# Kernel optimization log

Measured on AMD Instinct MI355X. Metric: run time of the kernel, lower is better.

Reference implementation:

```python
import jax, jax.numpy as jnp
import numpy as np
from jax import lax

B, S, W, V, E = 128, 128, 16, 128, 32
FILTERS = [256, 256, 256]
KS = [2, 3, 4]
NC = 10
EPS = 1e-5


def setup_inputs() -> dict:
    key = jax.random.key(0)
    ks = jax.random.split(key, 16)
    idx = jax.random.randint(ks[0], (B, S, W), 0, V)
    x = jax.nn.one_hot(idx, V, dtype=jnp.float32)  # [B,S,W,V] one-hot chars
    in_ch = E * W
    d = {"x": x, "emb_w": jax.random.normal(ks[1], (V, E), jnp.float32) * 0.05}
    for i, (f, k) in enumerate(zip(FILTERS, KS)):
        d[f"conv_w{i}"] = jax.random.normal(ks[2 + i], (f, in_ch, k), jnp.float32) * 0.02
        d[f"conv_b{i}"] = jnp.zeros((f,), jnp.float32)
        d[f"bn_g{i}"] = jnp.ones((f,), jnp.float32)
        d[f"bn_b{i}"] = jnp.zeros((f,), jnp.float32)
    d["fc1_w"] = jax.random.normal(ks[10], (sum(FILTERS), 100), jnp.float32) * 0.02
    d["fc1_b"] = jnp.zeros((100,), jnp.float32)
    d["bn1_g"] = jnp.ones((100,), jnp.float32)
    d["bn1_b"] = jnp.zeros((100,), jnp.float32)
    d["fc2_w"] = jax.random.normal(ks[11], (100, NC), jnp.float32) * 0.02
    d["fc2_b"] = jnp.zeros((NC,), jnp.float32)
    return d


def _bn(h, g, b, axes):
    # training-mode batchnorm with biased variance (matches torch BatchNorm math)
    mu = jnp.mean(h, axis=axes, keepdims=True)
    var = jnp.mean(jnp.square(h - mu), axis=axes, keepdims=True)
    shp = [1] * h.ndim
    shp[1] = h.shape[1]
    return (h - mu) * lax.rsqrt(var + EPS) * g.reshape(shp) + b.reshape(shp)


def _forward(x, emb_w, conv_ws, conv_bs, bn_gs, bn_bs, fc1_w, fc1_b, bn1_g, bn1_b, fc2_w, fc2_b):
    b, s, w, v = x.shape
    # one-hot bmm embedding == dense projection; flatten word_len*embed per word
    emb = jnp.einsum('bswv,ve->bswe', x, emb_w).reshape(b, s, w * emb_w.shape[1])
    h = emb.transpose(0, 2, 1)  # [B, W*E, S]
    pooled = []
    for cw, cb, g, bb in zip(conv_ws, conv_bs, bn_gs, bn_bs):
        c = lax.conv_general_dilated(h, cw, (1,), 'VALID',
                                     dimension_numbers=('NCH', 'OIH', 'NCH'))
        c = c + cb[None, :, None]
        c = jax.nn.relu(_bn(c, g, bb, axes=(0, 2)))
        pooled.append(jnp.max(c, axis=2))  # global max pool over length
    z = jnp.concatenate(pooled, axis=1)  # [B, sum(filters)]
    z = z @ fc1_w + fc1_b
    z = jax.nn.relu(_bn2d(z, bn1_g, bn1_b))
    # dropout is identity in eval mode
    return jax.nn.softmax(z @ fc2_w + fc2_b, axis=1)


def _bn2d(h, g, b):
    mu = jnp.mean(h, axis=0, keepdims=True)
    var = jnp.mean(jnp.square(h - mu), axis=0, keepdims=True)
    return (h - mu) * lax.rsqrt(var + EPS) * g[None, :] + b[None, :]


def reference(x, emb_w, conv_w0, conv_b0, bn_g0, bn_b0, conv_w1, conv_b1, bn_g1, bn_b1,
              conv_w2, conv_b2, bn_g2, bn_b2, fc1_w, fc1_b, bn1_g, bn1_b, fc2_w, fc2_b):
    return _forward(x, emb_w,
                    [conv_w0, conv_w1, conv_w2], [conv_b0, conv_b1, conv_b2],
                    [bn_g0, bn_g1, bn_g2], [bn_b0, bn_b1, bn_b2],
                    fc1_w, fc1_b, bn1_g, bn1_b, fc2_w, fc2_b)
```

## Files before the change

kernel.cpp:

```cpp
#include <hip/hip_runtime.h>
#include <cstdint>
#include <cstddef>

#define MTOT 16384
#define MPAD 16388
#define INCH 512
#define NF   256
#define PREPB 6144

typedef __attribute__((ext_vector_type(4))) float f32x4;
typedef __attribute__((ext_vector_type(8))) short bf16x8;

__device__ __forceinline__ short f2bf(float f) {
    union { float f; unsigned u; } v; v.f = f;
    unsigned r = v.u + 0x7FFFu + ((v.u >> 16) & 1u);
    return (short)(r >> 16);
}

__device__ __forceinline__ void gld16(const short* g, short* l) {
    __builtin_amdgcn_global_load_lds(
        (const __attribute__((address_space(1))) unsigned int*)g,
        (__attribute__((address_space(3))) unsigned int*)l,
        16, 0, 0);
}

__global__ void embed_prep(const float* __restrict__ x, const float* __restrict__ ew,
                           short* __restrict__ emb,
                           const float* __restrict__ w0, const float* __restrict__ w1,
                           const float* __restrict__ w2, short* __restrict__ Wtb) {
    int tid = threadIdx.x;
    if (blockIdx.x < PREPB) {
        int blk = blockIdx.x;
        int conv = blk >> 11;
        int ki = conv + 2;
        int K = 512 * ki;
        int idx = (blk & 2047) * 256 + tid;
        if (idx >= K * NF) return;
        int u = idx >> 9;
        int ic = idx & 511;
        int f = u / ki;
        int j = u - f * ki;
        const float* w = (conv == 0) ? w0 : (conv == 1) ? w1 : w2;
        float val = w[(size_t)f * K + ic * ki + j];
        int k = j * 512 + ic;
        int kt = k >> 6, kl = k & 63;
        int kc = kl >> 3, klo = kl & 7;
        int nb = f >> 7, fr = f & 127;
        int cc = kc ^ (fr & 7);
        size_t off = (conv == 0) ? 0 : (conv == 1) ? 262144 : 655360;
        Wtb[off + (((size_t)(kt * 2 + nb) * 128 + fr) * 8 + cc) * 8 + klo] = f2bf(val);
        return;
    }
    int m = blockIdx.x - PREPB;
    if (m >= MTOT) {
        if (tid < 64) {
            uint4 z = make_uint4(0u, 0u, 0u, 0u);
            *(uint4*)&emb[(size_t)m * INCH + tid * 8] = z;
        }
        return;
    }
    int w = tid >> 4, u = tid & 15;
    const float* xr = x + ((size_t)m * 16 + w) * 128 + u * 8;
    float4 a0 = *(const float4*)xr;
    float4 a1 = *(const float4*)(xr + 4);
    float vals[8] = {a0.x, a0.y, a0.z, a0.w, a1.x, a1.y, a1.z, a1.w};
    int myidx = 0;
#pragma unroll
    for (int jj = 0; jj < 8; ++jj)
        if (vals[jj] != 0.f) myidx = u * 8 + jj;
#pragma unroll
    for (int off = 1; off < 16; off <<= 1)
        myidx = max(myidx, __shfl_xor(myidx, off));
    if (u < 4) {
        const float* er = ew + (size_t)myidx * 32 + u * 8;
        float4 e0 = *(const float4*)er;
        float4 e1 = *(const float4*)(er + 4);
        short h[8];
        h[0] = f2bf(e0.x); h[1] = f2bf(e0.y); h[2] = f2bf(e0.z); h[3] = f2bf(e0.w);
        h[4] = f2bf(e1.x); h[5] = f2bf(e1.y); h[6] = f2bf(e1.z); h[7] = f2bf(e1.w);
        *(uint4*)&emb[(size_t)m * INCH + w * 32 + u * 8] = *(uint4*)h;
    }
}

__launch_bounds__(256)
__global__ void conv_gemm(const short* __restrict__ emb, const short* __restrict__ Wtb,
                          const float* __restrict__ cb0, const float* __restrict__ cb1,
                          const float* __restrict__ cb2,
                          float* __restrict__ sumP, float* __restrict__ ssqP,
                          float* __restrict__ mxF, float* __restrict__ mnF) {
    int o = blockIdx.x;
    int logical = (o & 7) * 96 + (o >> 3);
    int mb = logical / 6;
    int r6 = logical - mb * 6;
    int conv = r6 >> 1;
    int nb = r6 & 1;
    int ki = conv + 2;
    int m0 = mb * 128;
    const short* Wc = Wtb + ((conv == 0) ? 0 : (conv == 1) ? 262144 : 655360);

    __shared__ __align__(16) short As[128 * 64];
    __shared__ __align__(16) short Bs[128 * 64];

    int tid = threadIdx.x;
    int wv = tid >> 6, lane = tid & 63, g = lane >> 4, ln = lane & 15;
    int wr = wv >> 1, wc = wv & 1;

    f32x4 acc[4][4];
#pragma unroll
    for (int i = 0; i < 4; ++i)
#pragma unroll
        for (int n = 0; n < 4; ++n) acc[i][n] = (f32x4){0.f, 0.f, 0.f, 0.f};

    int arow[4], acol[4];
#pragma unroll
    for (int q = 0; q < 4; ++q) {
        int c = q * 256 + tid;
        arow[q] = c >> 3;
        acol[q] = ((c & 7) ^ (arow[q] & 7)) * 8;
    }
    int aOff[2][4], bOff[2][4];
#pragma unroll
    for (int kk = 0; kk < 2; ++kk)
#pragma unroll
        for (int i = 0; i < 4; ++i) {
            int R = wr * 64 + i * 16 + ln;
            aOff[kk][i] = R * 64 + (((kk * 4 + g) ^ (R & 7)) * 8);
            int F = wc * 64 + i * 16 + ln;
            bOff[kk][i] = F * 64 + (((kk * 4 + g) ^ (F & 7)) * 8);
        }

    for (int j = 0; j < ki; ++j) {
        const short* embj = emb + (size_t)(m0 + j) * INCH;
        for (int ic0 = 0; ic0 < INCH; ic0 += 64) {
            int kt = j * 8 + (ic0 >> 6);
            const short* Bsrc = Wc + (size_t)(kt * 2 + nb) * 8192;
            __syncthreads();
#pragma unroll
            for (int q = 0; q < 4; ++q) {
                gld16(embj + (size_t)arow[q] * INCH + ic0 + acol[q],
                      As + q * 2048 + wv * 512);
                gld16(Bsrc + (q * 256 + tid) * 8,
                      Bs + q * 2048 + wv * 512);
            }
            __syncthreads();
#pragma unroll
            for (int kk = 0; kk < 2; ++kk) {
                bf16x8 afr[4], bfr[4];
#pragma unroll
                for (int mi = 0; mi < 4; ++mi) afr[mi] = *(const bf16x8*)&As[aOff[kk][mi]];
#pragma unroll
                for (int ni = 0; ni < 4; ++ni) bfr[ni] = *(const bf16x8*)&Bs[bOff[kk][ni]];
#pragma unroll
                for (int mi = 0; mi < 4; ++mi)
#pragma unroll
                    for (int ni = 0; ni < 4; ++ni)
                        acc[mi][ni] = __builtin_amdgcn_mfma_f32_16x16x32_bf16(afr[mi], bfr[ni], acc[mi][ni], 0, 0, 0);
            }
        }
    }

    int L = 127 - conv;
    const float* cbp = (conv == 0) ? cb0 : (conv == 1) ? cb1 : cb2;
    float s[4] = {0.f, 0.f, 0.f, 0.f}, q[4] = {0.f, 0.f, 0.f, 0.f};
    float mx[4], mn[4], cb[4];
#pragma unroll
    for (int ni = 0; ni < 4; ++ni) {
        mx[ni] = -3.0e38f; mn[ni] = 3.0e38f;
        cb[ni] = cbp[nb * 128 + wc * 64 + ni * 16 + ln];
    }
#pragma unroll
    for (int mi = 0; mi < 4; ++mi) {
#pragma unroll
        for (int r = 0; r < 4; ++r) {
            int t = wr * 64 + mi * 16 + g * 4 + r;
            if (t >= L) continue;
#pragma unroll
            for (int ni = 0; ni < 4; ++ni) {
                float c = acc[mi][ni][r] + cb[ni];
                s[ni] += c; q[ni] += c * c;
                mx[ni] = fmaxf(mx[ni], c); mn[ni] = fminf(mn[ni], c);
            }
        }
    }
#pragma unroll
    for (int off = 16; off < 64; off <<= 1) {
#pragma unroll
        for (int ni = 0; ni < 4; ++ni) {
            s[ni] += __shfl_xor(s[ni], off);
            q[ni] += __shfl_xor(q[ni], off);
            mx[ni] = fmaxf(mx[ni], __shfl_xor(mx[ni], off));
            mn[ni] = fminf(mn[ni], __shfl_xor(mn[ni], off));
        }
    }
    __syncthreads();
    float* sm = (float*)As;
    if (g == 0) {
#pragma unroll
        for (int ni = 0; ni < 4; ++ni) {
            int col = wc * 64 + ni * 16 + ln;
            int oo = wr * 128 + col;
            sm[oo] = s[ni]; sm[256 + oo] = q[ni];
            sm[512 + oo] = mx[ni]; sm[768 + oo] = mn[ni];
        }
    }
    __syncthreads();
    if (tid < 128) {
        float S  = sm[tid] + sm[128 + tid];
        float Q  = sm[256 + tid] + sm[384 + tid];
        float MX = fmaxf(sm[512 + tid], sm[640 + tid]);
        float MN = fminf(sm[768 + tid], sm[896 + tid]);
        size_t off2 = ((size_t)(conv * 128 + mb)) * 256 + nb * 128 + tid;
        sumP[off2] = S; ssqP[off2] = Q; mxF[off2] = MX; mnF[off2] = MN;
    }
}

__global__ void bn_stats(const float* __restrict__ sumP, const float* __restrict__ ssqP,
                         const float* __restrict__ g0, const float* __restrict__ g1,
                         const float* __restrict__ g2,
                         const float* __restrict__ b0, const float* __restrict__ b1,
                         const float* __restrict__ b2,
                         float* __restrict__ af, float* __restrict__ df) {
    int conv = blockIdx.x;
    int tid = threadIdx.x;
    int part = tid >> 8, f = tid & 255;
    float s = 0.f, q = 0.f;
#pragma unroll 4
    for (int mb = part * 32; mb < part * 32 + 32; ++mb) {
        size_t o = ((size_t)(conv * 128 + mb)) * 256 + f;
        s += sumP[o]; q += ssqP[o];
    }
    __shared__ float sred[4][256], qred[4][256];
    sred[part][f] = s; qred[part][f] = q;
    __syncthreads();
    if (part == 0) {
        s = sred[0][f] + sred[1][f] + sred[2][f] + sred[3][f];
        q = qred[0][f] + qred[1][f] + qred[2][f] + qred[3][f];
        int L = 127 - conv;
        float n = 128.f * (float)L;
        float mu = s / n;
        float var = fmaxf(q / n - mu * mu, 0.f);
        const float* gp = (conv == 0) ? g0 : (conv == 1) ? g1 : g2;
        const float* bp = (conv == 0) ? b0 : (conv == 1) ? b1 : b2;
        float a = gp[f] * rsqrtf(var + 1e-5f);
        af[conv * 256 + f] = a;
        df[conv * 256 + f] = bp[f] - mu * a;
    }
}

__global__ void pool_fc1(const float* __restrict__ mxF, const float* __restrict__ mnF,
                         const float* __restrict__ af, const float* __restrict__ df,
                         const float* __restrict__ fc1w, const float* __restrict__ fc1b,
                         float* __restrict__ zb) {
    int b = blockIdx.x;
    int tid = threadIdx.x;
    __shared__ float pl[768];
    __shared__ float ps[8][100];
    if (tid < 768) {
        int conv = tid >> 8, f = tid & 255;
        size_t o = ((size_t)(conv * 128 + b)) * 256 + f;
        float a = af[tid], d = df[tid];
        float v = (a >= 0.f) ? mxF[o] : mnF[o];
        pl[tid] = fmaxf(a * v + d, 0.f);
    }
    __syncthreads();
    if (tid < 800) {
        int part = tid / 100, f = tid % 100;
        const float* pp = pl + part * 96;
        const float* wp = fc1w + (size_t)(part * 96) * 100 + f;
        float s = 0.f;
#pragma unroll 8
        for (int j = 0; j < 96; ++j) s += pp[j] * wp[(size_t)j * 100];
        ps[part][f] = s;
    }
    __syncthreads();
    if (tid < 100) {
        float s = fc1b[tid];
#pragma unroll
        for (int p = 0; p < 8; ++p) s += ps[p][tid];
        zb[b * 100 + tid] = s;
    }
}

__global__ void fc2bn_kernel(const float* __restrict__ zb, const float* __restrict__ g1,
                             const float* __restrict__ b1, const float* __restrict__ fc2w,
                             const float* __restrict__ fc2b, float* __restrict__ out) {
    int tid = threadIdx.x;
    __shared__ float z[128][101];
    __shared__ float av[100], dv[100];
    __shared__ float w2s[100][10];
    __shared__ float sst[8][100], qst[8][100];
    __shared__ float lgs[128][12];
    for (int i = tid; i < 12800; i += 1024) z[i / 100][i % 100] = zb[i];
    for (int i = tid; i < 1000; i += 1024) (&w2s[0][0])[i] = fc2w[i];
    __syncthreads();
    if (tid < 800) {
        int col = tid % 100, part = tid / 100;
        float s = 0.f, q = 0.f;
#pragma unroll 4
        for (int r = part * 16; r < part * 16 + 16; ++r) {
            float v = z[r][col]; s += v; q += v * v;
        }
        sst[part][col] = s; qst[part][col] = q;
    }
    __syncthreads();
    if (tid < 100) {
        float s = 0.f, q = 0.f;
#pragma unroll
        for (int p = 0; p < 8; ++p) { s += sst[p][tid]; q += qst[p][tid]; }
        float mu = s / 128.f;
        float var = fmaxf(q / 128.f - mu * mu, 0.f);
        float a = g1[tid] * rsqrtf(var + 1e-5f);
        av[tid] = a; dv[tid] = b1[tid] - mu * a;
    }
    __syncthreads();
    if (tid < 640) {
        int r = tid / 5, cg = tid % 5;
        int c0 = 2 * cg, c1 = c0 + 1;
        float l0 = fc2b[c0], l1 = fc2b[c1];
        for (int j = 0; j < 100; ++j) {
            float v = fmaxf(av[j] * z[r][j] + dv[j], 0.f);
            l0 += v * w2s[j][c0]; l1 += v * w2s[j][c1];
        }
        lgs[r][c0] = l0; lgs[r][c1] = l1;
    }
    __syncthreads();
    if (tid < 128) {
        int r = tid;
        float m = lgs[r][0];
#pragma unroll
        for (int c = 1; c < 10; ++c) m = fmaxf(m, lgs[r][c]);
        float e[10], sum = 0.f;
#pragma unroll
        for (int c = 0; c < 10; ++c) { e[c] = expf(lgs[r][c] - m); sum += e[c]; }
#pragma unroll
        for (int c = 0; c < 10; ++c) out[r * 10 + c] = e[c] / sum;
    }
}

extern "C" void kernel_launch(void* const* d_in, const int* in_sizes, int n_in,
                              void* d_out, int out_size, void* d_ws, size_t ws_size,
                              hipStream_t stream) {
    const float* x    = (const float*)d_in[0];
    const float* embw = (const float*)d_in[1];
    const float* cw0 = (const float*)d_in[2],  *cb0 = (const float*)d_in[3];
    const float* bg0 = (const float*)d_in[4],  *bb0 = (const float*)d_in[5];
    const float* cw1 = (const float*)d_in[6],  *cb1 = (const float*)d_in[7];
    const float* bg1 = (const float*)d_in[8],  *bb1 = (const float*)d_in[9];
    const float* cw2 = (const float*)d_in[10], *cb2 = (const float*)d_in[11];
    const float* bg2 = (const float*)d_in[12], *bb2 = (const float*)d_in[13];
    const float* fc1w = (const float*)d_in[14], *fc1b = (const float*)d_in[15];
    const float* g1   = (const float*)d_in[16], *b1   = (const float*)d_in[17];
    const float* fc2w = (const float*)d_in[18], *fc2b = (const float*)d_in[19];

    char* ws = (char*)d_ws;
    short* emb  = (short*)(ws);
    short* Wtb  = (short*)(ws + 16781312);
    float* sumP = (float*)(ws + 19140608);
    float* ssqP = (float*)(ws + 19533824);
    float* mxF  = (float*)(ws + 19927040);
    float* mnF  = (float*)(ws + 20320256);
    float* af   = (float*)(ws + 20713472);
    float* df   = (float*)(ws + 20716544);
    float* zb   = (float*)(ws + 20719616);

    embed_prep<<<PREPB + MPAD, 256, 0, stream>>>(x, embw, emb, cw0, cw1, cw2, Wtb);
    conv_gemm<<<768, 256, 0, stream>>>(emb, Wtb, cb0, cb1, cb2,
                                       sumP, ssqP, mxF, mnF);
    bn_stats<<<3, 1024, 0, stream>>>(sumP, ssqP, bg0, bg1, bg2, bb0, bb1, bb2, af, df);
    pool_fc1<<<128, 1024, 0, stream>>>(mxF, mnF, af, df, fc1w, fc1b, zb);
    fc2bn_kernel<<<1, 1024, 0, stream>>>(zb, g1, b1, fc2w, fc2b, (float*)d_out);
}
```

Measured before the change: 94.05 us.

## Reuse one A tile across all conv taps with K-chunk of 32

Restructures the conv GEMM loop so that each 32-wide input-channel chunk of the embedding is loaded once into shared memory (132 rows, covering the halo) and reused for every kernel tap by shifting the row index. Previously the A tile was reloaded from global memory for each tap. The weight layout and swizzle are changed to 32-wide K tiles to match, and the B tiles for all taps are loaded together. This cuts global/LDS traffic for A, but it halves the K per barrier pair, adds a scalar halo load from 16 threads, and uses a larger B shared buffer.

Result: no change. 92.61 us, median of 2 (-1.5%).

```diff
diff --git a/kernel.cpp b/kernel.cpp
--- a/kernel.cpp
+++ b/kernel.cpp
@@ -43,12 +43,12 @@
         const float* w = (conv == 0) ? w0 : (conv == 1) ? w1 : w2;
         float val = w[(size_t)f * K + ic * ki + j];
         int k = j * 512 + ic;
-        int kt = k >> 6, kl = k & 63;
+        int kt = k >> 5, kl = k & 31;
         int kc = kl >> 3, klo = kl & 7;
         int nb = f >> 7, fr = f & 127;
-        int cc = kc ^ (fr & 7);
+        int cc = kc ^ ((fr >> 1) & 3);
         size_t off = (conv == 0) ? 0 : (conv == 1) ? 262144 : 655360;
-        Wtb[off + (((size_t)(kt * 2 + nb) * 128 + fr) * 8 + cc) * 8 + klo] = f2bf(val);
+        Wtb[off + (((size_t)(kt * 2 + nb) * 128 + fr) * 4 + cc) * 8 + klo] = f2bf(val);
         return;
     }
     int m = blockIdx.x - PREPB;
@@ -98,8 +98,8 @@
     int m0 = mb * 128;
     const short* Wc = Wtb + ((conv == 0) ? 0 : (conv == 1) ? 262144 : 655360);
 
-    __shared__ __align__(16) short As[128 * 64];
-    __shared__ __align__(16) short Bs[128 * 64];
+    __shared__ __align__(16) short As[132 * 32];
+    __shared__ __align__(16) short Bs[4 * 4096];
 
     int tid = threadIdx.x;
     int wv = tid >> 6, lane = tid & 63, g = lane >> 4, ln = lane & 15;
@@ -111,51 +111,52 @@
 #pragma unroll
         for (int n = 0; n < 4; ++n) acc[i][n] = (f32x4){0.f, 0.f, 0.f, 0.f};
 
-    int arow[4], acol[4];
-#pragma unroll
-    for (int q = 0; q < 4; ++q) {
-        int c = q * 256 + tid;
-        arow[q] = c >> 3;
-        acol[q] = ((c & 7) ^ (arow[q] & 7)) * 8;
-    }
-    int aOff[2][4], bOff[2][4];
-#pragma unroll
-    for (int kk = 0; kk < 2; ++kk)
-#pragma unroll
-        for (int i = 0; i < 4; ++i) {
-            int R = wr * 64 + i * 16 + ln;
-            aOff[kk][i] = R * 64 + (((kk * 4 + g) ^ (R & 7)) * 8);
-            int F = wc * 64 + i * 16 + ln;
-            bOff[kk][i] = F * 64 + (((kk * 4 + g) ^ (F & 7)) * 8);
-        }
-
-    for (int j = 0; j < ki; ++j) {
-        const short* embj = emb + (size_t)(m0 + j) * INCH;
-        for (int ic0 = 0; ic0 < INCH; ic0 += 64) {
-            int kt = j * 8 + (ic0 >> 6);
-            const short* Bsrc = Wc + (size_t)(kt * 2 + nb) * 8192;
-            __syncthreads();
-#pragma unroll
-            for (int q = 0; q < 4; ++q) {
-                gld16(embj + (size_t)arow[q] * INCH + ic0 + acol[q],
-                      As + q * 2048 + wv * 512);
-                gld16(Bsrc + (q * 256 + tid) * 8,
-                      Bs + q * 2048 + wv * 512);
+    int arow0 = tid >> 2, acol0 = (((tid)&3) ^ ((arow0 >> 1) & 3)) * 8;
+    int arow1 = (256 + tid) >> 2, acol1 = (((256 + tid) & 3) ^ ((arow1 >> 1) & 3)) * 8;
+    int xrow = 128 + (tid >> 2);
+    int xcol = (((tid) & 3) ^ ((xrow >> 1) & 3)) * 8;
+    int c0 = tid, c1 = 256 + tid;
+
+    int bOff[4];
+#pragma unroll
+    for (int i = 0; i < 4; ++i) {
+        int F = wc * 64 + i * 16 + ln;
+        bOff[i] = F * 32 + ((g ^ ((F >> 1) & 3)) * 8);
+    }
+    int Rb[4];
+#pragma unroll
+    for (int i = 0; i < 4; ++i) Rb[i] = wr * 64 + i * 16 + ln;
+
+    for (int ic0 = 0; ic0 < INCH; ic0 += 32) {
+        int kt0 = ic0 >> 5;
+        const short* abase = emb + (size_t)m0 * INCH + ic0;
+        __syncthreads();
+        gld16(abase + (size_t)arow0 * INCH + acol0, As + wv * 512);
+        gld16(abase + (size_t)arow1 * INCH + acol1, As + 2048 + wv * 512);
+        if (tid < 16) {
+            bf16x8 v = *(const bf16x8*)&abase[(size_t)xrow * INCH + xcol];
+            *(bf16x8*)&As[(512 + tid) * 8] = v;
+        }
+        for (int jj = 0; jj < ki; ++jj) {
+            const short* Bsrc = Wc + (size_t)((jj * 16 + kt0) * 2 + nb) * 4096;
+            gld16(Bsrc + c0 * 8, Bs + jj * 4096 + wv * 512);
+            gld16(Bsrc + c1 * 8, Bs + jj * 4096 + 2048 + wv * 512);
+        }
+        __syncthreads();
+        for (int jj = 0; jj < ki; ++jj) {
+            bf16x8 afr[4], bfr[4];
+#pragma unroll
+            for (int i = 0; i < 4; ++i) {
+                int Rj = Rb[i] + jj;
+                afr[i] = *(const bf16x8*)&As[Rj * 32 + ((g ^ ((Rj >> 1) & 3)) * 8)];
             }
-            __syncthreads();
-#pragma unroll
-            for (int kk = 0; kk < 2; ++kk) {
-                bf16x8 afr[4], bfr[4];
-#pragma unroll
-                for (int mi = 0; mi < 4; ++mi) afr[mi] = *(const bf16x8*)&As[aOff[kk][mi]];
-#pragma unroll
-                for (int ni = 0; ni < 4; ++ni) bfr[ni] = *(const bf16x8*)&Bs[bOff[kk][ni]];
-#pragma unroll
-                for (int mi = 0; mi < 4; ++mi)
-#pragma unroll
-                    for (int ni = 0; ni < 4; ++ni)
-                        acc[mi][ni] = __builtin_amdgcn_mfma_f32_16x16x32_bf16(afr[mi], bfr[ni], acc[mi][ni], 0, 0, 0);
-            }
+#pragma unroll
+            for (int i = 0; i < 4; ++i) bfr[i] = *(const bf16x8*)&Bs[jj * 4096 + bOff[i]];
+#pragma unroll
+            for (int mi = 0; mi < 4; ++mi)
+#pragma unroll
+                for (int ni = 0; ni < 4; ++ni)
+                    acc[mi][ni] = __builtin_amdgcn_mfma_f32_16x16x32_bf16(afr[mi], bfr[ni], acc[mi][ni], 0, 0, 0);
         }
     }
 
```
